# Kernel optimization log

Hardware: AMD Instinct MI355X
Metric: run time of the kernel (lower is better)

## Reference

```python
import jax, jax.numpy as jnp
import numpy as np

DIM_E, DIM_M, DIM_C = 1024, 64, 128
B, N = 4, 4096


def setup_inputs() -> dict:
    key = jax.random.key(0)
    ks = jax.random.split(key, 10)
    s = 1.0 / np.sqrt(DIM_E + DIM_C)
    return {
        "e": jax.random.normal(ks[0], (B, N, DIM_E), jnp.float32),
        "m": jax.random.normal(ks[1], (B, N, DIM_M), jnp.float32),
        "c": jax.random.normal(ks[2], (B, N, DIM_C), jnp.float32),
        "l": jax.random.uniform(ks[3], (B, N), jnp.float32),
        "Wq": jax.random.uniform(ks[4], (DIM_E + DIM_C, DIM_E), jnp.float32, -s, s),
        "bq": jax.random.uniform(ks[5], (DIM_E,), jnp.float32, -s, s),
        "Wk": jax.random.uniform(ks[6], (DIM_E + DIM_C, DIM_E), jnp.float32, -s, s),
        "bk": jax.random.uniform(ks[7], (DIM_E,), jnp.float32, -s, s),
        "Wv": jax.random.uniform(ks[8], (DIM_E + DIM_C, DIM_E), jnp.float32, -s, s),
        "bv": jax.random.uniform(ks[9], (DIM_E,), jnp.float32, -s, s),
    }


def reference(e, m, c, l, Wq, bq, Wk, bk, Wv, bv):
    x = jnp.concatenate([e, c], axis=-1)                       # [B,N,De+Dc]
    q = jnp.einsum('bnd,df->bnf', x, Wq) + bq                  # [B,N,De]
    k = jnp.einsum('bnd,df->bnf', x, Wk) + bk
    v = jnp.einsum('bnd,df->bnf', x, Wv) + bv
    scale = 1.0 / jnp.sqrt(jnp.asarray(q.shape[-1], q.dtype))
    attn_scores = jnp.einsum('bqd,bkd->bqk', q, k) * scale     # [B,N,N]
    membrane_mask = jnp.einsum('bqm,bkm->bqk', m, m)           # [B,N,N]
    lifespan_mask = l[:, :, None] * l[:, None, :]              # [B,N,N]
    adaptive_scores = attn_scores * membrane_mask * lifespan_mask
    attn_weights = jax.nn.softmax(adaptive_scores, axis=-1)
    h_tilde = jnp.einsum('bqk,bkd->bqd', attn_weights, v)      # [B,N,De]
    e_new = e + h_tilde
    return (e_new, h_tilde)
```

## Files before the change

### kernel.cpp

```cpp
#include <hip/hip_runtime.h>
#include <hip/hip_bf16.h>

#define DE 1024
#define DM 64
#define DC 128
#define DX 1152
#define NB 4
#define NN 4096
#define NT 16384

typedef _Float16 f16;
typedef _Float16 f16x4 __attribute__((ext_vector_type(4)));
typedef _Float16 f16x8 __attribute__((ext_vector_type(8)));
typedef float f32x4 __attribute__((ext_vector_type(4)));

__device__ __forceinline__ void g2l16(const void* g, void* l) {
  __builtin_amdgcn_global_load_lds(
      (const __attribute__((address_space(1))) unsigned int*)(unsigned long long)g,
      (__attribute__((address_space(3))) unsigned int*)(unsigned int)(unsigned long long)l,
      16, 0, 0);
}

#define SBAR() do { __builtin_amdgcn_sched_barrier(0);                 \
                    __builtin_amdgcn_s_barrier();                      \
                    __builtin_amdgcn_sched_barrier(0); } while (0)
#define VMWAIT(n) do { asm volatile("s_waitcnt vmcnt(" #n ")");        \
                       __builtin_amdgcn_sched_barrier(0); } while (0)

__global__ void build_x_kernel(const float* __restrict__ e, const float* __restrict__ c,
                               f16* __restrict__ Xb) {
  const int total = NT * DX / 4;
  for (int i = blockIdx.x * blockDim.x + threadIdx.x; i < total; i += gridDim.x * blockDim.x) {
    int idx = i * 4;
    int r = idx / DX, col = idx - r * DX;
    float4 v;
    if (col < DE) v = *(const float4*)(e + (long)r * DE + col);
    else          v = *(const float4*)(c + (long)r * DC + (col - DE));
    f16x4 o = { (f16)v.x, (f16)v.y, (f16)v.z, (f16)v.w };
    *(f16x4*)(Xb + (long)idx) = o;
  }
}

__global__ void conv_f16_kernel(const float* __restrict__ in, f16* __restrict__ out, int total4) {
  for (int i = blockIdx.x * blockDim.x + threadIdx.x; i < total4; i += gridDim.x * blockDim.x) {
    float4 v = *(const float4*)(in + (long)i * 4);
    f16x4 o = { (f16)v.x, (f16)v.y, (f16)v.z, (f16)v.w };
    *(f16x4*)(out + (long)i * 4) = o;
  }
}

__global__ void transpose_w_kernel(const float* __restrict__ in, f16* __restrict__ out) {
  __shared__ float tile[32][33];
  int c0 = blockIdx.x * 32, r0 = blockIdx.y * 32;
  int x = threadIdx.x, y = threadIdx.y;
#pragma unroll
  for (int i = 0; i < 4; ++i)
    tile[y + 8 * i][x] = in[(long)(r0 + y + 8 * i) * DE + (c0 + x)];
  __syncthreads();
#pragma unroll
  for (int i = 0; i < 4; ++i)
    out[(long)(c0 + y + 8 * i) * DX + (r0 + x)] = (f16)tile[x][y + 8 * i];
}

__device__ __forceinline__ void mm_loop(const f16* __restrict__ A, const f16* __restrict__ B,
                                        int lda, int ldb, int K,
                                        f16* lA, f16* lB, f32x4 (&acc)[4][4]) {
  const int t = threadIdx.x;
  const int lane = t & 63;
  const int wid = t >> 6;
  const int wr = (wid >> 1) * 64, wc = (wid & 1) * 64;
  const int fr = lane & 15, fq = lane >> 4;
  for (int k0 = 0; k0 < K; k0 += 32) {
    __syncthreads();
#pragma unroll
    for (int it = 0; it < 2; ++it) {
      int byteoff = it * 4096 + t * 16;
      int row = byteoff >> 6;
      int ke = (byteoff & 63) >> 1;
      g2l16(A + (long)row * lda + k0 + ke, lA + (byteoff >> 1));
      g2l16(B + (long)row * ldb + k0 + ke, lB + (byteoff >> 1));
    }
    __syncthreads();
    f16x8 af[4], bfr[4];
#pragma unroll
    for (int i = 0; i < 4; ++i) {
      af[i]  = *(const f16x8*)(lA + (wr + i * 16 + fr) * 32 + fq * 8);
      bfr[i] = *(const f16x8*)(lB + (wc + i * 16 + fr) * 32 + fq * 8);
    }
#pragma unroll
    for (int m = 0; m < 4; ++m)
#pragma unroll
      for (int n = 0; n < 4; ++n)
        acc[m][n] = __builtin_amdgcn_mfma_f32_16x16x32_f16(af[m], bfr[n], acc[m][n], 0, 0, 0);
  }
}

__global__ __launch_bounds__(256) void mask_kernel(
    const f16* __restrict__ mb, const float* __restrict__ l, f16* __restrict__ Pm) {
  __shared__ __attribute__((aligned(16))) f16 lA[128 * 32], lB[128 * 32];
  f32x4 acc[4][4];
#pragma unroll
  for (int m = 0; m < 4; ++m)
#pragma unroll
    for (int n = 0; n < 4; ++n) acc[m][n] = (f32x4){0.f, 0.f, 0.f, 0.f};
  const int b = blockIdx.z;
  const int row0 = blockIdx.x * 128, col0 = blockIdx.y * 128;
  mm_loop(mb + (long)(b * NN + row0) * DM, mb + (long)(b * NN + col0) * DM,
          DM, DM, DM, lA, lB, acc);
  const int lane = threadIdx.x & 63, wid = threadIdx.x >> 6;
  const int wr = (wid >> 1) * 64, wc = (wid & 1) * 64;
  const int fr = lane & 15, fq = lane >> 4;
  const float* lb = l + (long)b * NN;
  f16* out = Pm + (long)b * NN * NN;
#pragma unroll
  for (int n = 0; n < 4; ++n) {
    int col = col0 + wc + n * 16 + fr;
    float lc = lb[col] * 0.03125f;
#pragma unroll
    for (int m = 0; m < 4; ++m)
#pragma unroll
      for (int r = 0; r < 4; ++r) {
        int row = row0 + wr + m * 16 + fq * 4 + r;
        out[(long)row * NN + col] = (f16)(acc[m][n][r] * lc * lb[row]);
      }
  }
}

__device__ __forceinline__ void gemm8_core(
    const f16* __restrict__ A, long lda,
    const f16* __restrict__ B, long ldb,
    int NTt, char* ldsb, f32x4 (&acc)[8][4]) {
  const int tid = threadIdx.x;
  const int lane = tid & 63, wid = tid >> 6;
  const int wr = wid >> 2, wc = wid & 3;
  const int fr = lane & 15, fq = lane >> 4;
  const int cb0 = ((fq) ^ (fr & 7)) << 4;
  const int cb1 = ((4 | fq) ^ (fr & 7)) << 4;

  auto stageA = [&](int pc, int kt, int par) {
    char* base = ldsb + par * 32768;
    int k0 = kt * 64;
#pragma unroll
    for (int it = 0; it < 2; ++it) {
      int p = it * 8192 + tid * 16;
      int off = pc * 8192 + ((p >> 13) << 14) + (p & 8191);
      int sw = off ^ (((off >> 7) & 7) << 4);
      int row = sw >> 7;
      int colf = ((sw >> 4) & 7) << 3;
      g2l16(A + (long)row * lda + k0 + colf, base + off);
    }
  };
  auto stageB = [&](int pc, int kt, int par) {
    char* base = ldsb + 65536 + par * 32768;
    int k0 = kt * 64;
#pragma unroll
    for (int it = 0; it < 2; ++it) {
      int p = it * 8192 + tid * 16;
      int off = pc * 4096 + ((p >> 12) << 13) + (p & 4095);
      int sw = off ^ (((off >> 7) & 7) << 4);
      int row = sw >> 7;
      int colf = ((sw >> 4) & 7) << 3;
      g2l16(B + (long)row * ldb + k0 + colf, base + off);
    }
  };

  f16x8 af[4][2], bf0[2][2], bf1[2][2];
  auto rdA = [&](int mh, int par) {
    const char* base = ldsb + par * 32768;
#pragma unroll
    for (int i = 0; i < 4; ++i) {
      int row = wr * 128 + mh * 64 + i * 16 + fr;
      af[i][0] = *(const f16x8*)(const void*)(base + row * 128 + cb0);
      af[i][1] = *(const f16x8*)(const void*)(base + row * 128 + cb1);
    }
  };
  auto rdB = [&](f16x8 (&bf)[2][2], int nh, int par) {
    const char* base = ldsb + 65536 + par * 32768;
#pragma unroll
    for (int i = 0; i < 2; ++i) {
      int row = wc * 64 + nh * 32 + i * 16 + fr;
      bf[i][0] = *(const f16x8*)(const void*)(base + row * 128 + cb0);
      bf[i][1] = *(const f16x8*)(const void*)(base + row * 128 + cb1);
    }
  };
  auto mma = [&](f16x8 (&bf)[2][2], int mo, int no) {
    __builtin_amdgcn_s_setprio(1);
#pragma unroll
    for (int k = 0; k < 2; ++k)
#pragma unroll
      for (int m = 0; m < 4; ++m)
#pragma unroll
        for (int n = 0; n < 2; ++n)
          acc[mo + m][no + n] =
              __builtin_amdgcn_mfma_f32_16x16x32_f16(af[m][k], bf[n][k], acc[mo + m][no + n], 0, 0, 0);
    __builtin_amdgcn_s_setprio(0);
  };

  stageA(0, 0, 0); stageB(0, 0, 0); stageA(1, 0, 0); stageB(1, 0, 0);
  stageA(0, 1, 1); stageB(0, 1, 1); stageA(1, 1, 1); stageB(1, 1, 1);
  VMWAIT(8);
  SBAR();

  for (int t = 0; t < NTt; t += 2) {
#pragma unroll
    for (int half = 0; half < 2; ++half) {
      const int tt = t + half;
      const int par = half;
      rdA(0, par); rdB(bf0, 0, par);
      SBAR();
      mma(bf0, 0, 0);
      SBAR();
      rdB(bf1, 1, par);
      if (tt + 2 < NTt) stageA(0, tt + 2, par);
      SBAR();
      mma(bf1, 0, 2);
      SBAR();
      rdA(1, par);
      if (tt + 2 < NTt) stageB(0, tt + 2, par);
      SBAR();
      mma(bf1, 4, 2);
      SBAR();
      if (tt + 2 < NTt) {
        stageA(1, tt + 2, par); stageB(1, tt + 2, par);
        VMWAIT(8);
      } else if (tt + 1 < NTt) {
        VMWAIT(0);
      }
      SBAR();
      mma(bf0, 4, 0);
      SBAR();
    }
  }
}

__device__ __forceinline__ void swz_grid(int& bx, int& by, int& bz) {
  int nx = gridDim.x, ny = gridDim.y;
  int flat = blockIdx.x + nx * (blockIdx.y + ny * blockIdx.z);
  int total = nx * ny * gridDim.z;
  int cpx = total >> 3;
  flat = (flat & 7) * cpx + (flat >> 3);
  bx = flat % nx; int r = flat / nx;
  by = r % ny; bz = r / ny;
}

#define ACC_INIT()                                                  \
  f32x4 acc[8][4];                                                  \
  _Pragma("unroll") for (int m_ = 0; m_ < 8; ++m_)                  \
  _Pragma("unroll") for (int n_ = 0; n_ < 4; ++n_)                  \
      acc[m_][n_] = (f32x4){0.f, 0.f, 0.f, 0.f};

#define EPI8_IDX()                                                  \
  const int lane = threadIdx.x & 63, wid = threadIdx.x >> 6;        \
  const int wr = wid >> 2, wc = wid & 3;                            \
  const int fr = lane & 15, fq = lane >> 4;

__global__ __launch_bounds__(512, 2) void qk8_kernel(
    const f16* __restrict__ Xb, const f16* __restrict__ Wt,
    const float* __restrict__ bq, const float* __restrict__ bk,
    f16* __restrict__ qb, f16* __restrict__ kb) {
  __shared__ __attribute__((aligned(128))) char ldsb[131072];
  int bx, by, bz; swz_grid(bx, by, bz);
  const int row0 = bx * 256, col0 = by * 256;
  ACC_INIT();
  gemm8_core(Xb + (long)row0 * DX, DX, Wt + (long)col0 * DX, DX, DX / 64, ldsb, acc);
  EPI8_IDX();
  const bool isq = col0 < DE;
  const float* bvec = isq ? bq : bk;
  f16* ob = isq ? qb : kb;
  const int cbase = (isq ? col0 : col0 - DE) + wc * 64;
  const int rbase = row0 + wr * 128;
#pragma unroll
  for (int n = 0; n < 4; ++n) {
    int col = cbase + n * 16 + fr;
    float bb = bvec[col];
#pragma unroll
    for (int m = 0; m < 8; ++m)
#pragma unroll
      for (int j = 0; j < 4; ++j) {
        int row = rbase + m * 16 + fq * 4 + j;
        ob[(long)row * DE + col] = (f16)(acc[m][n][j] + bb);
      }
  }
}

__global__ __launch_bounds__(512, 2) void vt8_kernel(
    const f16* __restrict__ WtV, const f16* __restrict__ Xb,
    const float* __restrict__ bv, f16* __restrict__ Vt) {
  __shared__ __attribute__((aligned(128))) char ldsb[131072];
  int bx, by, bz; swz_grid(bx, by, bz);
  const int row0 = bx * 256, col0 = by * 256;
  ACC_INIT();
  gemm8_core(WtV + (long)row0 * DX, DX, Xb + (long)col0 * DX, DX, DX / 64, ldsb, acc);
  EPI8_IDX();
  const int cbase = col0 + wc * 64;
  const int rbase = row0 + wr * 128;
#pragma unroll
  for (int n = 0; n < 4; ++n) {
    int col = cbase + n * 16 + fr;
#pragma unroll
    for (int m = 0; m < 8; ++m)
#pragma unroll
      for (int j = 0; j < 4; ++j) {
        int row = rbase + m * 16 + fq * 4 + j;
        Vt[(long)row * NT + col] = (f16)(acc[m][n][j] + bv[row]);
      }
  }
}

__global__ __launch_bounds__(512, 2) void sc8_kernel(
    const f16* __restrict__ qb_, const f16* __restrict__ kb_, float* __restrict__ S) {
  __shared__ __attribute__((aligned(128))) char ldsb[131072];
  int bx, by, bz; swz_grid(bx, by, bz);
  const int row0 = bx * 256, col0 = by * 256;
  ACC_INIT();
  gemm8_core(qb_ + (long)row0 * DE, DE, kb_ + (long)col0 * DE, DE, DE / 64, ldsb, acc);
  EPI8_IDX();
  const int cbase = col0 + wc * 64;
  const int rbase = row0 + wr * 128;
#pragma unroll
  for (int n = 0; n < 4; ++n) {
    int col = cbase + n * 16 + fr;
#pragma unroll
    for (int m = 0; m < 8; ++m)
#pragma unroll
      for (int j = 0; j < 4; ++j) {
        int row = rbase + m * 16 + fq * 4 + j;
        S[(long)row * NN + col] = acc[m][n][j];
      }
  }
}

__global__ __launch_bounds__(512, 2) void pv8_kernel(
    const f16* __restrict__ P, const f16* __restrict__ Vt,
    const float* __restrict__ e, float* __restrict__ outE, float* __restrict__ outH) {
  __shared__ __attribute__((aligned(128))) char ldsb[131072];
  int bx, by, bz; swz_grid(bx, by, bz);
  const int b = bz;
  const int row0 = bx * 256, col0 = by * 256;
  ACC_INIT();
  gemm8_core(P + (long)b * NN * NN + (long)row0 * NN, NN,
             Vt + (long)col0 * NT + (long)b * NN, NT, NN / 64, ldsb, acc);
  EPI8_IDX();
  const int cbase = col0 + wc * 64;
  const int rbase = row0 + wr * 128;
#pragma unroll
  for (int n = 0; n < 4; ++n) {
    int col = cbase + n * 16 + fr;
#pragma unroll
    for (int m = 0; m < 8; ++m)
#pragma unroll
      for (int j = 0; j < 4; ++j) {
        int row = rbase + m * 16 + fq * 4 + j;
        long idx = ((long)b * NN + row) * DE + col;
        float h = acc[m][n][j];
        outE[idx] = e[idx] + h;
        outH[idx] = h;
      }
  }
}

__global__ __launch_bounds__(256) void softmax_kernel(const float* __restrict__ S,
                                                      const f16* __restrict__ Pm,
                                                      f16* __restrict__ P) {
  __shared__ float red[8];
  const long row = blockIdx.x;
  const float* s = S + row * NN;
  const f16* pmr = Pm + row * NN;
  const int t = threadIdx.x;
  float4 v[4];
  float mx = -3.0e38f;
#pragma unroll
  for (int i = 0; i < 4; ++i) {
    v[i] = *(const float4*)(s + t * 4 + i * 1024);
    f16x4 m4 = *(const f16x4*)(pmr + t * 4 + i * 1024);
    v[i].x *= (float)m4[0]; v[i].y *= (float)m4[1];
    v[i].z *= (float)m4[2]; v[i].w *= (float)m4[3];
    mx = fmaxf(mx, fmaxf(fmaxf(v[i].x, v[i].y), fmaxf(v[i].z, v[i].w)));
  }
#pragma unroll
  for (int o = 32; o; o >>= 1) mx = fmaxf(mx, __shfl_xor(mx, o));
  if ((t & 63) == 0) red[t >> 6] = mx;
  __syncthreads();
  mx = fmaxf(fmaxf(red[0], red[1]), fmaxf(red[2], red[3]));
  float sum = 0.f;
#pragma unroll
  for (int i = 0; i < 4; ++i) {
    v[i].x = __expf(v[i].x - mx); v[i].y = __expf(v[i].y - mx);
    v[i].z = __expf(v[i].z - mx); v[i].w = __expf(v[i].w - mx);
    sum += v[i].x + v[i].y + v[i].z + v[i].w;
  }
#pragma unroll
  for (int o = 32; o; o >>= 1) sum += __shfl_xor(sum, o);
  if ((t & 63) == 0) red[4 + (t >> 6)] = sum;
  __syncthreads();
  float inv = 1.f / (red[4] + red[5] + red[6] + red[7]);
  f16* p = P + row * NN;
#pragma unroll
  for (int i = 0; i < 4; ++i) {
    f16x4 o4 = { (f16)(v[i].x * inv), (f16)(v[i].y * inv),
                 (f16)(v[i].z * inv), (f16)(v[i].w * inv) };
    *(f16x4*)(p + t * 4 + i * 1024) = o4;
  }
}

extern "C" void kernel_launch(void* const* d_in, const int* in_sizes, int n_in,
                              void* d_out, int out_size, void* d_ws, size_t ws_size,
                              hipStream_t stream) {
  const float* e  = (const float*)d_in[0];
  const float* m  = (const float*)d_in[1];
  const float* c  = (const float*)d_in[2];
  const float* l  = (const float*)d_in[3];
  const float* Wq = (const float*)d_in[4];
  const float* bq = (const float*)d_in[5];
  const float* Wk = (const float*)d_in[6];
  const float* bk = (const float*)d_in[7];
  const float* Wv = (const float*)d_in[8];
  const float* bv = (const float*)d_in[9];
  float* outE = (float*)d_out;
  float* outH = outE + (long)NT * DE;

  char* ws = (char*)d_ws;
  size_t off = 0;
  auto alloc = [&](size_t bytes) {
    char* p = ws + off;
    off += (bytes + 255) & ~(size_t)255;
    return p;
  };
  f16* Xb    = (f16*)alloc((size_t)NT * DX * 2);
  f16* WtQK  = (f16*)alloc((size_t)2048 * DX * 2);
  f16* WtV   = (f16*)alloc((size_t)DE * DX * 2);
  f16* qb    = (f16*)alloc((size_t)NT * DE * 2);
  f16* kb    = (f16*)alloc((size_t)NT * DE * 2);
  f16* Vt    = (f16*)alloc((size_t)DE * NT * 2);
  f16* mb    = (f16*)alloc((size_t)NT * DM * 2);
  float* S   = (float*)alloc((size_t)NN * NN * 4);
  f16* P     = (f16*)alloc((size_t)NB * NN * NN * 2);
  if (off > ws_size) return;

  build_x_kernel<<<2048, 256, 0, stream>>>(e, c, Xb);
  conv_f16_kernel<<<512, 256, 0, stream>>>(m, mb, NT * DM / 4);
  transpose_w_kernel<<<dim3(32, 36), dim3(32, 8), 0, stream>>>(Wq, WtQK);
  transpose_w_kernel<<<dim3(32, 36), dim3(32, 8), 0, stream>>>(Wk, WtQK + (size_t)DE * DX);
  transpose_w_kernel<<<dim3(32, 36), dim3(32, 8), 0, stream>>>(Wv, WtV);
  mask_kernel<<<dim3(32, 32, NB), 256, 0, stream>>>(mb, l, P);
  qk8_kernel<<<dim3(64, 8), 512, 0, stream>>>(Xb, WtQK, bq, bk, qb, kb);
  vt8_kernel<<<dim3(4, 64), 512, 0, stream>>>(WtV, Xb, bv, Vt);
  for (int b = 0; b < NB; ++b) {
    sc8_kernel<<<dim3(16, 16), 512, 0, stream>>>(
        qb + (size_t)b * NN * DE, kb + (size_t)b * NN * DE, S);
    softmax_kernel<<<NN, 256, 0, stream>>>(S, P + (size_t)b * NN * NN, P + (size_t)b * NN * NN);
  }
  pv8_kernel<<<dim3(16, 4, NB), 512, 0, stream>>>(P, Vt, e, outE, outH);
}
```

Baseline: 679.8 us.

## Replace 256x256 8-wave GEMM core with 256x128 4-wave K32 double-buffered core

Swaps the shared GEMM mainloop from a 512-thread, 256x256 tile with 64-deep K steps and a swizzled 128 KB LDS buffer for a 256-thread, 256x128 tile. The new loop uses 32-deep K steps, an unswizzled 48 KB double buffer and a simpler read/MFMA/stage schedule with an explicit lgkmcnt wait. All four GEMM kernels and their grids are retiled to match. The smaller LDS footprint may allow more blocks per CU and more tiles, at the cost of lower operand reuse per tile and possible LDS bank conflicts from dropping the XOR swizzle.

```diff
diff --git a/kernel.cpp b/kernel.cpp
--- a/kernel.cpp
+++ b/kernel.cpp
@@ -24,8 +24,12 @@
 #define SBAR() do { __builtin_amdgcn_sched_barrier(0);                 \
                     __builtin_amdgcn_s_barrier();                      \
                     __builtin_amdgcn_sched_barrier(0); } while (0)
-#define VMWAIT(n) do { asm volatile("s_waitcnt vmcnt(" #n ")");        \
+#define VMWAIT(n) do { __builtin_amdgcn_sched_barrier(0);              \
+                       asm volatile("s_waitcnt vmcnt(" #n ")");        \
                        __builtin_amdgcn_sched_barrier(0); } while (0)
+#define LGKM0() do { __builtin_amdgcn_sched_barrier(0);                \
+                     asm volatile("s_waitcnt lgkmcnt(0)");             \
+                     __builtin_amdgcn_sched_barrier(0); } while (0)
 
 __global__ void build_x_kernel(const float* __restrict__ e, const float* __restrict__ c,
                                f16* __restrict__ Xb) {
@@ -126,110 +130,74 @@
   }
 }
 
-__device__ __forceinline__ void gemm8_core(
+__device__ __forceinline__ void gemm4_core(
     const f16* __restrict__ A, long lda,
     const f16* __restrict__ B, long ldb,
     int NTt, char* ldsb, f32x4 (&acc)[8][4]) {
   const int tid = threadIdx.x;
   const int lane = tid & 63, wid = tid >> 6;
-  const int wr = wid >> 2, wc = wid & 3;
+  const int wr = wid >> 1, wc = wid & 1;
   const int fr = lane & 15, fq = lane >> 4;
-  const int cb0 = ((fq) ^ (fr & 7)) << 4;
-  const int cb1 = ((4 | fq) ^ (fr & 7)) << 4;
-
-  auto stageA = [&](int pc, int kt, int par) {
-    char* base = ldsb + par * 32768;
-    int k0 = kt * 64;
-#pragma unroll
-    for (int it = 0; it < 2; ++it) {
-      int p = it * 8192 + tid * 16;
-      int off = pc * 8192 + ((p >> 13) << 14) + (p & 8191);
-      int sw = off ^ (((off >> 7) & 7) << 4);
-      int row = sw >> 7;
-      int colf = ((sw >> 4) & 7) << 3;
-      g2l16(A + (long)row * lda + k0 + colf, base + off);
-    }
+
+  const f16* srcA = A + (long)(tid >> 2) * lda + (tid & 3) * 8;
+  const f16* srcB = B + (long)(tid >> 2) * ldb + (tid & 3) * 8;
+
+  auto stageA = [&](int kt, int par) {
+    char* base = ldsb + par * 24576;
+#pragma unroll
+    for (int it = 0; it < 4; ++it)
+      g2l16(srcA + (long)(it * 64) * lda + kt * 32, base + it * 4096 + tid * 16);
   };
-  auto stageB = [&](int pc, int kt, int par) {
-    char* base = ldsb + 65536 + par * 32768;
-    int k0 = kt * 64;
-#pragma unroll
-    for (int it = 0; it < 2; ++it) {
-      int p = it * 8192 + tid * 16;
-      int off = pc * 4096 + ((p >> 12) << 13) + (p & 4095);
-      int sw = off ^ (((off >> 7) & 7) << 4);
-      int row = sw >> 7;
-      int colf = ((sw >> 4) & 7) << 3;
-      g2l16(B + (long)row * ldb + k0 + colf, base + off);
-    }
+  auto stageB = [&](int kt, int par) {
+    char* base = ldsb + par * 24576 + 16384;
+#pragma unroll
+    for (int it = 0; it < 2; ++it)
+      g2l16(srcB + (long)(it * 64) * ldb + kt * 32, base + it * 4096 + tid * 16);
   };
 
-  f16x8 af[4][2], bf0[2][2], bf1[2][2];
-  auto rdA = [&](int mh, int par) {
-    const char* base = ldsb + par * 32768;
-#pragma unroll
-    for (int i = 0; i < 4; ++i) {
-      int row = wr * 128 + mh * 64 + i * 16 + fr;
-      af[i][0] = *(const f16x8*)(const void*)(base + row * 128 + cb0);
-      af[i][1] = *(const f16x8*)(const void*)(base + row * 128 + cb1);
-    }
-  };
-  auto rdB = [&](f16x8 (&bf)[2][2], int nh, int par) {
-    const char* base = ldsb + 65536 + par * 32768;
-#pragma unroll
-    for (int i = 0; i < 2; ++i) {
-      int row = wc * 64 + nh * 32 + i * 16 + fr;
-      bf[i][0] = *(const f16x8*)(const void*)(base + row * 128 + cb0);
-      bf[i][1] = *(const f16x8*)(const void*)(base + row * 128 + cb1);
-    }
-  };
-  auto mma = [&](f16x8 (&bf)[2][2], int mo, int no) {
+  const int aoff = (wr * 128 + fr) * 64 + fq * 16;
+  const int boff = (wc * 64 + fr) * 64 + fq * 16;
+
+  auto mma16 = [&](f16x8 (&a4)[4], f16x8 (&b4)[4], int mo) {
     __builtin_amdgcn_s_setprio(1);
 #pragma unroll
-    for (int k = 0; k < 2; ++k)
-#pragma unroll
-      for (int m = 0; m < 4; ++m)
-#pragma unroll
-        for (int n = 0; n < 2; ++n)
-          acc[mo + m][no + n] =
-              __builtin_amdgcn_mfma_f32_16x16x32_f16(af[m][k], bf[n][k], acc[mo + m][no + n], 0, 0, 0);
+    for (int m = 0; m < 4; ++m)
+#pragma unroll
+      for (int n = 0; n < 4; ++n)
+        acc[mo + m][n] =
+            __builtin_amdgcn_mfma_f32_16x16x32_f16(a4[m], b4[n], acc[mo + m][n], 0, 0, 0);
     __builtin_amdgcn_s_setprio(0);
   };
 
-  stageA(0, 0, 0); stageB(0, 0, 0); stageA(1, 0, 0); stageB(1, 0, 0);
-  stageA(0, 1, 1); stageB(0, 1, 1); stageA(1, 1, 1); stageB(1, 1, 1);
-  VMWAIT(8);
+  stageA(0, 0); stageB(0, 0); stageA(1, 1); stageB(1, 1);
+  VMWAIT(6);
   SBAR();
 
-  for (int t = 0; t < NTt; t += 2) {
-#pragma unroll
-    for (int half = 0; half < 2; ++half) {
-      const int tt = t + half;
-      const int par = half;
-      rdA(0, par); rdB(bf0, 0, par);
-      SBAR();
-      mma(bf0, 0, 0);
-      SBAR();
-      rdB(bf1, 1, par);
-      if (tt + 2 < NTt) stageA(0, tt + 2, par);
-      SBAR();
-      mma(bf1, 0, 2);
-      SBAR();
-      rdA(1, par);
-      if (tt + 2 < NTt) stageB(0, tt + 2, par);
-      SBAR();
-      mma(bf1, 4, 2);
-      SBAR();
-      if (tt + 2 < NTt) {
-        stageA(1, tt + 2, par); stageB(1, tt + 2, par);
-        VMWAIT(8);
-      } else if (tt + 1 < NTt) {
-        VMWAIT(0);
-      }
-      SBAR();
-      mma(bf0, 4, 0);
-      SBAR();
+  for (int tt = 0; tt < NTt; ++tt) {
+    const int par = tt & 1;
+    const char* bA = ldsb + par * 24576;
+    const char* bB = bA + 16384;
+    f16x8 af[4], af2[4], bf[4];
+#pragma unroll
+    for (int i = 0; i < 4; ++i)
+      af[i] = *(const f16x8*)(const void*)(bA + aoff + i * 1024);
+#pragma unroll
+    for (int n = 0; n < 4; ++n)
+      bf[n] = *(const f16x8*)(const void*)(bB + boff + n * 1024);
+    mma16(af, bf, 0);
+#pragma unroll
+    for (int i = 0; i < 4; ++i)
+      af2[i] = *(const f16x8*)(const void*)(bA + aoff + 4096 + i * 1024);
+    LGKM0();
+    SBAR();
+    mma16(af2, bf, 4);
+    if (tt + 2 < NTt) {
+      stageA(tt + 2, par); stageB(tt + 2, par);
+      VMWAIT(6);
+    } else {
+      VMWAIT(0);
     }
+    SBAR();
   }
 }
 
@@ -249,21 +217,21 @@
   _Pragma("unroll") for (int n_ = 0; n_ < 4; ++n_)                  \
       acc[m_][n_] = (f32x4){0.f, 0.f, 0.f, 0.f};
 
-#define EPI8_IDX()                                                  \
+#define EPI4_IDX()                                                  \
   const int lane = threadIdx.x & 63, wid = threadIdx.x >> 6;        \
-  const int wr = wid >> 2, wc = wid & 3;                            \
+  const int wr = wid >> 1, wc = wid & 1;                            \
   const int fr = lane & 15, fq = lane >> 4;
 
-__global__ __launch_bounds__(512, 2) void qk8_kernel(
+__global__ __launch_bounds__(256, 2) void qk8_kernel(
     const f16* __restrict__ Xb, const f16* __restrict__ Wt,
     const float* __restrict__ bq, const float* __restrict__ bk,
     f16* __restrict__ qb, f16* __restrict__ kb) {
-  __shared__ __attribute__((aligned(128))) char ldsb[131072];
+  __shared__ __attribute__((aligned(128))) char ldsb[49152];
   int bx, by, bz; swz_grid(bx, by, bz);
-  const int row0 = bx * 256, col0 = by * 256;
+  const int row0 = bx * 256, col0 = by * 128;
   ACC_INIT();
-  gemm8_core(Xb + (long)row0 * DX, DX, Wt + (long)col0 * DX, DX, DX / 64, ldsb, acc);
-  EPI8_IDX();
+  gemm4_core(Xb + (long)row0 * DX, DX, Wt + (long)col0 * DX, DX, DX / 32, ldsb, acc);
+  EPI4_IDX();
   const bool isq = col0 < DE;
   const float* bvec = isq ? bq : bk;
   f16* ob = isq ? qb : kb;
@@ -283,15 +251,15 @@
   }
 }
 
-__global__ __launch_bounds__(512, 2) void vt8_kernel(
+__global__ __launch_bounds__(256, 2) void vt8_kernel(
     const f16* __restrict__ WtV, const f16* __restrict__ Xb,
     const float* __restrict__ bv, f16* __restrict__ Vt) {
-  __shared__ __attribute__((aligned(128))) char ldsb[131072];
+  __shared__ __attribute__((aligned(128))) char ldsb[49152];
   int bx, by, bz; swz_grid(bx, by, bz);
-  const int row0 = bx * 256, col0 = by * 256;
+  const int row0 = bx * 256, col0 = by * 128;
   ACC_INIT();
-  gemm8_core(WtV + (long)row0 * DX, DX, Xb + (long)col0 * DX, DX, DX / 64, ldsb, acc);
-  EPI8_IDX();
+  gemm4_core(WtV + (long)row0 * DX, DX, Xb + (long)col0 * DX, DX, DX / 32, ldsb, acc);
+  EPI4_IDX();
   const int cbase = col0 + wc * 64;
   const int rbase = row0 + wr * 128;
 #pragma unroll
@@ -307,14 +275,14 @@
   }
 }
 
-__global__ __launch_bounds__(512, 2) void sc8_kernel(
+__global__ __launch_bounds__(256, 2) void sc8_kernel(
     const f16* __restrict__ qb_, const f16* __restrict__ kb_, float* __restrict__ S) {
-  __shared__ __attribute__((aligned(128))) char ldsb[131072];
+  __shared__ __attribute__((aligned(128))) char ldsb[49152];
   int bx, by, bz; swz_grid(bx, by, bz);
-  const int row0 = bx * 256, col0 = by * 256;
+  const int row0 = bx * 256, col0 = by * 128;
   ACC_INIT();
-  gemm8_core(qb_ + (long)row0 * DE, DE, kb_ + (long)col0 * DE, DE, DE / 64, ldsb, acc);
-  EPI8_IDX();
+  gemm4_core(qb_ + (long)row0 * DE, DE, kb_ + (long)col0 * DE, DE, DE / 32, ldsb, acc);
+  EPI4_IDX();
   const int cbase = col0 + wc * 64;
   const int rbase = row0 + wr * 128;
 #pragma unroll
@@ -330,17 +298,17 @@
   }
 }
 
-__global__ __launch_bounds__(512, 2) void pv8_kernel(
+__global__ __launch_bounds__(256, 2) void pv8_kernel(
     const f16* __restrict__ P, const f16* __restrict__ Vt,
     const float* __restrict__ e, float* __restrict__ outE, float* __restrict__ outH) {
-  __shared__ __attribute__((aligned(128))) char ldsb[131072];
+  __shared__ __attribute__((aligned(128))) char ldsb[49152];
   int bx, by, bz; swz_grid(bx, by, bz);
   const int b = bz;
-  const int row0 = bx * 256, col0 = by * 256;
+  const int row0 = bx * 256, col0 = by * 128;
   ACC_INIT();
-  gemm8_core(P + (long)b * NN * NN + (long)row0 * NN, NN,
-             Vt + (long)col0 * NT + (long)b * NN, NT, NN / 64, ldsb, acc);
-  EPI8_IDX();
+  gemm4_core(P + (long)b * NN * NN + (long)row0 * NN, NN,
+             Vt + (long)col0 * NT + (long)b * NN, NT, NN / 32, ldsb, acc);
+  EPI4_IDX();
   const int cbase = col0 + wc * 64;
   const int rbase = row0 + wr * 128;
 #pragma unroll
@@ -443,12 +411,12 @@
   transpose_w_kernel<<<dim3(32, 36), dim3(32, 8), 0, stream>>>(Wk, WtQK + (size_t)DE * DX);
   transpose_w_kernel<<<dim3(32, 36), dim3(32, 8), 0, stream>>>(Wv, WtV);
   mask_kernel<<<dim3(32, 32, NB), 256, 0, stream>>>(mb, l, P);
-  qk8_kernel<<<dim3(64, 8), 512, 0, stream>>>(Xb, WtQK, bq, bk, qb, kb);
-  vt8_kernel<<<dim3(4, 64), 512, 0, stream>>>(WtV, Xb, bv, Vt);
+  qk8_kernel<<<dim3(64, 16), 256, 0, stream>>>(Xb, WtQK, bq, bk, qb, kb);
+  vt8_kernel<<<dim3(4, 128), 256, 0, stream>>>(WtV, Xb, bv, Vt);
   for (int b = 0; b < NB; ++b) {
-    sc8_kernel<<<dim3(16, 16), 512, 0, stream>>>(
+    sc8_kernel<<<dim3(16, 32), 256, 0, stream>>>(
         qb + (size_t)b * NN * DE, kb + (size_t)b * NN * DE, S);
     softmax_kernel<<<NN, 256, 0, stream>>>(S, P + (size_t)b * NN * NN, P + (size_t)b * NN * NN);
   }
-  pv8_kernel<<<dim3(16, 4, NB), 512, 0, stream>>>(P, Vt, e, outE, outH);
-}
+  pv8_kernel<<<dim3(16, 8, NB), 256, 0, stream>>>(P, Vt, e, outE, outH);
+}
```

After: 782.9 us. 1.15x slower.

## Prefetch next K-tile LDS fragments into double-buffered registers during final MMA

Applied to the files above, without the earlier changes.

Restructures the GEMM main loop so the LDS fragment reads for the next K-tile (A first half and B first half) are issued before the last MMA group of the current tile. Ping-pong register sets hold them, and the first fragments are loaded before the loop. This hides LDS read latency behind MFMA work. It also changes the barrier macros, dropping the sched_barrier that preceded s_barrier and moving it ahead of the vmcnt wait. The extra live fragment registers raise register pressure and may reduce occupancy or cause spills.

```diff
diff --git a/kernel.cpp b/kernel.cpp
--- a/kernel.cpp
+++ b/kernel.cpp
@@ -21,11 +21,12 @@
       16, 0, 0);
 }
 
-#define SBAR() do { __builtin_amdgcn_sched_barrier(0);                 \
-                    __builtin_amdgcn_s_barrier();                      \
+#define BARS() do { __builtin_amdgcn_s_barrier();                      \
                     __builtin_amdgcn_sched_barrier(0); } while (0)
-#define VMWAIT(n) do { asm volatile("s_waitcnt vmcnt(" #n ")");        \
-                       __builtin_amdgcn_sched_barrier(0); } while (0)
+#define VMW8() do { __builtin_amdgcn_sched_barrier(0);                 \
+                    asm volatile("s_waitcnt vmcnt(8)"); } while (0)
+#define VMW0() do { __builtin_amdgcn_sched_barrier(0);                 \
+                    asm volatile("s_waitcnt vmcnt(0)"); } while (0)
 
 __global__ void build_x_kernel(const float* __restrict__ e, const float* __restrict__ c,
                                f16* __restrict__ Xb) {
@@ -164,26 +165,25 @@
     }
   };
 
-  f16x8 af[4][2], bf0[2][2], bf1[2][2];
-  auto rdA = [&](int mh, int par) {
+  auto rdA2 = [&](f16x8 (&a)[4][2], int mh, int i0, int par) {
     const char* base = ldsb + par * 32768;
 #pragma unroll
-    for (int i = 0; i < 4; ++i) {
+    for (int i = i0; i < i0 + 2; ++i) {
       int row = wr * 128 + mh * 64 + i * 16 + fr;
-      af[i][0] = *(const f16x8*)(const void*)(base + row * 128 + cb0);
-      af[i][1] = *(const f16x8*)(const void*)(base + row * 128 + cb1);
-    }
-  };
-  auto rdB = [&](f16x8 (&bf)[2][2], int nh, int par) {
+      a[i][0] = *(const f16x8*)(const void*)(base + row * 128 + cb0);
+      a[i][1] = *(const f16x8*)(const void*)(base + row * 128 + cb1);
+    }
+  };
+  auto rdB = [&](f16x8 (&b)[2][2], int nh, int par) {
     const char* base = ldsb + 65536 + par * 32768;
 #pragma unroll
     for (int i = 0; i < 2; ++i) {
       int row = wc * 64 + nh * 32 + i * 16 + fr;
-      bf[i][0] = *(const f16x8*)(const void*)(base + row * 128 + cb0);
-      bf[i][1] = *(const f16x8*)(const void*)(base + row * 128 + cb1);
-    }
-  };
-  auto mma = [&](f16x8 (&bf)[2][2], int mo, int no) {
+      b[i][0] = *(const f16x8*)(const void*)(base + row * 128 + cb0);
+      b[i][1] = *(const f16x8*)(const void*)(base + row * 128 + cb1);
+    }
+  };
+  auto mma = [&](f16x8 (&a)[4][2], f16x8 (&b)[2][2], int mo, int no) {
     __builtin_amdgcn_s_setprio(1);
 #pragma unroll
     for (int k = 0; k < 2; ++k)
@@ -192,44 +192,54 @@
 #pragma unroll
         for (int n = 0; n < 2; ++n)
           acc[mo + m][no + n] =
-              __builtin_amdgcn_mfma_f32_16x16x32_f16(af[m][k], bf[n][k], acc[mo + m][no + n], 0, 0, 0);
+              __builtin_amdgcn_mfma_f32_16x16x32_f16(a[m][k], b[n][k], acc[mo + m][no + n], 0, 0, 0);
     __builtin_amdgcn_s_setprio(0);
+  };
+
+  f16x8 a0A[4][2], b0A[2][2], a0B[4][2], b0B[2][2];
+
+  auto body = [&](f16x8 (&a0)[4][2], f16x8 (&b0)[2][2],
+                  f16x8 (&a0n)[4][2], f16x8 (&b0n)[2][2],
+                  int par, int tt) {
+    const int npar = par ^ 1;
+    f16x8 a1[4][2], b1[2][2];
+    rdB(b1, 1, par);
+    BARS();
+    mma(a0, b0, 0, 0);
+    BARS();
+    rdA2(a1, 1, 0, par); rdA2(a1, 1, 2, par);
+    if (tt + 2 < NTt) stageA(0, tt + 2, par);
+    BARS();
+    mma(a0, b1, 0, 2);
+    BARS();
+    if (tt + 2 < NTt) stageB(0, tt + 2, par);
+    BARS();
+    mma(a1, b1, 4, 2);
+    BARS();
+    if (tt + 2 < NTt) {
+      stageA(1, tt + 2, par); stageB(1, tt + 2, par);
+      VMW8();
+    } else if (tt + 1 < NTt) {
+      VMW0();
+    }
+    if (tt + 1 < NTt) {
+      rdB(b0n, 0, npar);
+      rdA2(a0n, 0, 0, npar); rdA2(a0n, 0, 2, npar);
+    }
+    BARS();
+    mma(a1, b0, 4, 0);
+    BARS();
   };
 
   stageA(0, 0, 0); stageB(0, 0, 0); stageA(1, 0, 0); stageB(1, 0, 0);
   stageA(0, 1, 1); stageB(0, 1, 1); stageA(1, 1, 1); stageB(1, 1, 1);
-  VMWAIT(8);
-  SBAR();
+  VMW8();
+  BARS();
+  rdB(b0A, 0, 0); rdA2(a0A, 0, 0, 0); rdA2(a0A, 0, 2, 0);
 
   for (int t = 0; t < NTt; t += 2) {
-#pragma unroll
-    for (int half = 0; half < 2; ++half) {
-      const int tt = t + half;
-      const int par = half;
-      rdA(0, par); rdB(bf0, 0, par);
-      SBAR();
-      mma(bf0, 0, 0);
-      SBAR();
-      rdB(bf1, 1, par);
-      if (tt + 2 < NTt) stageA(0, tt + 2, par);
-      SBAR();
-      mma(bf1, 0, 2);
-      SBAR();
-      rdA(1, par);
-      if (tt + 2 < NTt) stageB(0, tt + 2, par);
-      SBAR();
-      mma(bf1, 4, 2);
-      SBAR();
-      if (tt + 2 < NTt) {
-        stageA(1, tt + 2, par); stageB(1, tt + 2, par);
-        VMWAIT(8);
-      } else if (tt + 1 < NTt) {
-        VMWAIT(0);
-      }
-      SBAR();
-      mma(bf0, 4, 0);
-      SBAR();
-    }
+    body(a0A, b0A, a0B, b0B, 0, t);
+    body(a0B, b0B, a0A, b0A, 1, t + 1);
   }
 }
 
```

Result: slower. 2.116 ms (+211.2%).
